# Kernel optimization log

Hardware: AMD Instinct MI355X
Metric: run time of the kernel (lower is better)

## Reference

```python
import jax, jax.numpy as jnp
import numpy as np

EPS = 1e-8

def setup_inputs() -> dict:
    key = jax.random.key(0)
    k1, k2 = jax.random.split(key)
    B, C, T_text, max_len = 16, 256, 512, 4096
    x = jax.random.normal(k1, (B, C, T_text), dtype=jnp.float32)
    # positive linear-domain durations, mean ~ max_len / T_text = 8
    w = jax.random.uniform(k2, (B, T_text), dtype=jnp.float32) * 16.0
    x_mask = jnp.ones((B, 1, T_text), dtype=jnp.float32)
    y_mask = jnp.ones((B, 1, max_len), dtype=jnp.float32)
    sigma_scale = jnp.ones((1,), dtype=jnp.float32)
    return {"x": x, "w": w, "x_mask": x_mask, "y_mask": y_mask, "sigma_scale": sigma_scale}

def reference(x, w, x_mask, y_mask, sigma_scale):
    # x: (B, C, T_text), w: (B, T_text), y_mask: (B, 1, max_len)
    x = x * x_mask
    center = jnp.cumsum(w, axis=1) - 0.5 * w            # (B, T_text)
    max_len = y_mask.shape[2]
    pos = jnp.arange(max_len, dtype=x.dtype)            # (max_len,)
    mu = pos[None, None, :] - center[:, :, None]        # (B, T_text, max_len)
    sigma = w[:, :, None] * sigma_scale[0]              # (B, T_text, 1)
    weights = jnp.exp(-0.5 * jnp.square(mu) / (jnp.square(sigma) + EPS))
    weights = weights / (jnp.sum(weights, axis=1, keepdims=True) + EPS)
    upsampled = jnp.einsum('bct,btl->bcl', x, weights)  # (B, C, max_len)
    return upsampled * y_mask
```

## Files before the change

### kernel.cpp

```cpp
#include <hip/hip_runtime.h>
#include <hip/hip_bf16.h>

#define EPS 1e-8f

#define BB 16
#define CC 256
#define TT 512
#define LL 4096
#define KC  32
#define TCB 128
#define TLB 64
#define XR  40

typedef __attribute__((ext_vector_type(8))) short short8;
typedef __attribute__((ext_vector_type(4))) float f32x4;

__device__ __forceinline__ unsigned short bfbits(float f) {
    __hip_bfloat16 h = __float2bfloat16(f);
    return *(unsigned short*)&h;
}
__device__ __forceinline__ unsigned int pack2(float lo, float hi) {
    return (unsigned int)bfbits(lo) | ((unsigned int)bfbits(hi) << 16);
}

__global__ __launch_bounds__(512)
void scan_kernel(const float* __restrict__ w,
                 const float* __restrict__ sigma_scale,
                 float* __restrict__ center,
                 float* __restrict__ nhis,
                 float* __restrict__ delta) {
    const int b = blockIdx.x;
    const int t = threadIdx.x;
    const int lane = t & 63;
    const int wid  = t >> 6;
    __shared__ float part[8], offs[8], wmx[8];

    const float wv = w[b * TT + t];
    float v = wv;
#pragma unroll
    for (int o = 1; o < 64; o <<= 1) {
        float u = __shfl_up(v, o);
        if (lane >= o) v += u;
    }
    float m = wv;
#pragma unroll
    for (int o = 1; o < 64; o <<= 1) m = fmaxf(m, __shfl_xor(m, o));
    if (lane == 63) part[wid] = v;
    if (lane == 0)  wmx[wid] = m;
    __syncthreads();
    const float ss = sigma_scale[0];
    if (t == 0) {
        float run = 0.0f, mm = 0.0f;
#pragma unroll
        for (int i = 0; i < 8; ++i) {
            offs[i] = run;
            run += part[i];
            mm = fmaxf(mm, wmx[i]);
        }
        delta[b] = 8.0f * (mm * ss + 1e-4f) + 1.0f;
    }
    __syncthreads();
    v += offs[wid];
    center[b * TT + t] = v - 0.5f * wv;
    const float sg = wv * ss;
    nhis[b * TT + t] = -0.5f / (sg * sg + EPS);
}


#define ISSUE(tc_)                                                              \
    {                                                                           \
        _Pragma("unroll")                                                       \
        for (int i = 0; i < 4; ++i) {                                           \
            const int idx4 = tid + 256 * i;                                     \
            const int c    = idx4 >> 3;                                         \
            const int t4   = idx4 & 7;                                          \
            gx[i] = *(const float4*)&x[xbase + (size_t)c * TT + (tc_) + t4 * 4];\
        }                                                                       \
    }

#define WRITEX(buf_)                                                            \
    {                                                                           \
        _Pragma("unroll")                                                       \
        for (int i = 0; i < 4; ++i) {                                           \
            const int idx4 = tid + 256 * i;                                     \
            const int c    = idx4 >> 3;                                         \
            const int t4   = idx4 & 7;                                          \
            ushort4 v4;                                                         \
            v4.x = bfbits(gx[i].x);                                             \
            v4.y = bfbits(gx[i].y);                                             \
            v4.z = bfbits(gx[i].z);                                             \
            v4.w = bfbits(gx[i].w);                                             \
            *(ushort4*)&xs[buf_][c][t4 * 4] = v4;                               \
        }                                                                       \
    }

#define EXPW(tc_, buf_)                                                         \
    {                                                                           \
        _Pragma("unroll")                                                       \
        for (int i = 0; i < 2; ++i) {                                           \
            const int slot  = tid + 256 * i;                                    \
            const int l_loc = slot >> 3;                                        \
            const int t4    = slot & 7;                                         \
            const int t0    = (tc_) + t4 * 4;                                   \
            const float4 cv = *(const float4*)&center[bTT + t0];                \
            const float4 nv = *(const float4*)&nhis[bTT + t0];                  \
            const float4 xm = *(const float4*)&x_mask[bTT + t0];                \
            const float posf = (float)(l0 + l_loc);                             \
            float mu, e0, e1, e2, e3;                                           \
            mu = posf - cv.x; e0 = __expf(mu * mu * nv.x);                      \
            mu = posf - cv.y; e1 = __expf(mu * mu * nv.y);                      \
            mu = posf - cv.z; e2 = __expf(mu * mu * nv.z);                      \
            mu = posf - cv.w; e3 = __expf(mu * mu * nv.w);                      \
            const float ps = (e0 + e1) + (e2 + e3);                             \
            if (i == 0) p0 += ps; else p1 += ps;                                \
            uint2 pk;                                                           \
            pk.x = pack2(e0 * xm.x, e1 * xm.y);                                 \
            pk.y = pack2(e2 * xm.z, e3 * xm.w);                                 \
            *(uint2*)&ws[buf_][l_loc][t4 * 4] = pk;                             \
        }                                                                       \
    }

#define MFMA_STEP(buf_)                                                         \
    {                                                                           \
        short8 af[2], bfr[4];                                                   \
        _Pragma("unroll")                                                       \
        for (int m = 0; m < 2; ++m)                                             \
            af[m] = *(const short8*)&xs[buf_][wv * 32 + m * 16 + lq][lg * 8];   \
        _Pragma("unroll")                                                       \
        for (int n = 0; n < 4; ++n)                                             \
            bfr[n] = *(const short8*)&ws[buf_][n * 16 + lq][lg * 8];            \
        _Pragma("unroll")                                                       \
        for (int m = 0; m < 2; ++m)                                             \
            _Pragma("unroll")                                                   \
            for (int n = 0; n < 4; ++n)                                         \
                acc[m][n] = __builtin_amdgcn_mfma_f32_16x16x32_bf16(            \
                    af[m], bfr[n], acc[m][n], 0, 0, 0);                         \
    }

__global__ __launch_bounds__(256, 4)
void fused_kernel(const float* __restrict__ x,
                  const float* __restrict__ x_mask,
                  const float* __restrict__ y_mask,
                  const float* __restrict__ center,
                  const float* __restrict__ nhis,
                  const float* __restrict__ delta,
                  float* __restrict__ out) {
    __shared__ unsigned short xs[2][TCB][XR];
    __shared__ unsigned short ws[2][TLB][XR];
    __shared__ float dsum[TLB];
    __shared__ float sscale[TLB];
    __shared__ int tmin_s, tmax_s;

    const int gid = blockIdx.x;
    const int lid = (gid & 7) * 256 + (gid >> 3);
    const int b   = lid >> 7;
    const int rr_ = lid & 127;
    const int l0  = (rr_ >> 1) * TLB;
    const int c0  = (rr_ & 1) * TCB;

    const int tid  = threadIdx.x;
    const int lane = tid & 63;
    const int wv   = tid >> 6;
    const int lq   = lane & 15;
    const int lg   = lane >> 4;
    const int bTT  = b * TT;
    const size_t xbase = (size_t)(b * CC + c0) * TT;

    if (tid == 0) { tmin_s = TT; tmax_s = -1; }
    __syncthreads();
    const float D  = delta[b];
    const float lo = (float)l0 - D;
    const float hi = (float)(l0 + TLB - 1) + D;
#pragma unroll
    for (int i = 0; i < 2; ++i) {
        const int tt = tid + 256 * i;
        const float c = center[bTT + tt];
        if (c >= lo && c <= hi) {
            atomicMin(&tmin_s, tt);
            atomicMax(&tmax_s, tt);
        }
    }
    __syncthreads();
    const int tlo = tmin_s & ~(KC - 1);
    const int nch = (tmax_s >= 0) ? ((((tmax_s & ~(KC - 1)) + KC) - tlo) / KC) : 0;

    f32x4 acc[2][4];
#pragma unroll
    for (int m = 0; m < 2; ++m)
#pragma unroll
        for (int n = 0; n < 4; ++n) acc[m][n] = (f32x4)0.0f;
    float p0 = 0.0f, p1 = 0.0f;

    float4 gx[4];

    if (nch > 0) {
        ISSUE(tlo);
        EXPW(tlo, 0);
        WRITEX(0);
        __syncthreads();
        for (int i = 0; i < nch; ++i) {
            const int cur = i & 1;
            const int tc1 = tlo + (i + 1) * KC;
            if (i + 1 < nch) {
                ISSUE(tc1);
                EXPW(tc1, cur ^ 1);
            }
            MFMA_STEP(cur);
            if (i + 1 < nch) WRITEX(cur ^ 1);
            __syncthreads();
        }
    }

#pragma unroll
    for (int o = 1; o < 8; o <<= 1) {
        p0 += __shfl_xor(p0, o);
        p1 += __shfl_xor(p1, o);
    }
    if ((tid & 7) == 0) {
        dsum[tid >> 3]        = p0;
        dsum[(tid >> 3) + 32] = p1;
    }
    __syncthreads();
    if (tid < TLB)
        sscale[tid] = y_mask[b * LL + l0 + tid] / (dsum[tid] + EPS);
    __syncthreads();

    float sc[4];
#pragma unroll
    for (int n = 0; n < 4; ++n) sc[n] = sscale[n * 16 + lq];

    const size_t obase = (size_t)(b * CC + c0) * LL + l0;
#pragma unroll
    for (int m = 0; m < 2; ++m) {
#pragma unroll
        for (int r = 0; r < 4; ++r) {
            const int c = wv * 32 + m * 16 + lg * 4 + r;
            float* op = &out[obase + (size_t)c * LL];
#pragma unroll
            for (int n = 0; n < 4; ++n)
                op[n * 16 + lq] = acc[m][n][r] * sc[n];
        }
    }
}

extern "C" void kernel_launch(void* const* d_in, const int* in_sizes, int n_in,
                              void* d_out, int out_size, void* d_ws, size_t ws_size,
                              hipStream_t stream) {
    const float* x           = (const float*)d_in[0];
    const float* w           = (const float*)d_in[1];
    const float* x_mask      = (const float*)d_in[2];
    const float* y_mask      = (const float*)d_in[3];
    const float* sigma_scale = (const float*)d_in[4];
    float* out = (float*)d_out;

    float* center = (float*)d_ws;
    float* nhis   = center + BB * TT;
    float* delta  = nhis + BB * TT;

    hipLaunchKernelGGL(scan_kernel, dim3(BB), dim3(512), 0, stream,
                       w, sigma_scale, center, nhis, delta);
    hipLaunchKernelGGL(fused_kernel, dim3((LL / TLB) * (CC / TCB) * BB), dim3(256), 0, stream,
                       x, x_mask, y_mask, center, nhis, delta, out);
}
```

Before: 28.30 us.

## Fuse scan into main kernel, widen L tile, load x fragments directly from global

Drops the separate scan kernel: each block recomputes the prefix sum, centers, inverse variances and delta for its batch row in shared memory, removing one launch and the global round trip for the intermediates. The L tile doubles to 128, so each wave holds 16 accumulators and the grid halves. The x tile is no longer staged through shared memory; each lane reads its MFMA A fragment straight from global memory and converts it to bf16. The risks are redundant scan work in every block, more register pressure, and exposed global-load latency inside the MFMA loop.

Result: faster. 24.29 us (-14.2%).

```diff
diff --git a/kernel.cpp b/kernel.cpp
--- a/kernel.cpp
+++ b/kernel.cpp
@@ -9,7 +9,7 @@
 #define LL 4096
 #define KC  32
 #define TCB 128
-#define TLB 64
+#define TLB 128
 #define XR  40
 
 typedef __attribute__((ext_vector_type(8))) short short8;
@@ -23,223 +23,191 @@
     return (unsigned int)bfbits(lo) | ((unsigned int)bfbits(hi) << 16);
 }
 
-__global__ __launch_bounds__(512)
-void scan_kernel(const float* __restrict__ w,
-                 const float* __restrict__ sigma_scale,
-                 float* __restrict__ center,
-                 float* __restrict__ nhis,
-                 float* __restrict__ delta) {
-    const int b = blockIdx.x;
-    const int t = threadIdx.x;
-    const int lane = t & 63;
-    const int wid  = t >> 6;
-    __shared__ float part[8], offs[8], wmx[8];
-
-    const float wv = w[b * TT + t];
-    float v = wv;
+
+#define EXPW(tc_, buf_)                                                         \
+    {                                                                           \
+        _Pragma("unroll")                                                       \
+        for (int i_ = 0; i_ < 2; ++i_) {                                        \
+            const int slot  = tid + 256 * i_;                                   \
+            const int l_loc = slot >> 2;                                        \
+            const int tg    = slot & 3;                                         \
+            const int t0    = (tc_) + tg * 8;                                   \
+            const float4 cv0 = *(const float4*)&cen_s[t0];                      \
+            const float4 cv1 = *(const float4*)&cen_s[t0 + 4];                  \
+            const float4 nv0 = *(const float4*)&nh_s[t0];                       \
+            const float4 nv1 = *(const float4*)&nh_s[t0 + 4];                   \
+            const float4 xk0 = *(const float4*)&xm_s[t0];                       \
+            const float4 xk1 = *(const float4*)&xm_s[t0 + 4];                   \
+            const float posf = (float)(l0 + l_loc);                             \
+            float mu, e0, e1, e2, e3, e4, e5, e6, e7;                           \
+            mu = posf - cv0.x; e0 = __expf(mu * mu * nv0.x);                    \
+            mu = posf - cv0.y; e1 = __expf(mu * mu * nv0.y);                    \
+            mu = posf - cv0.z; e2 = __expf(mu * mu * nv0.z);                    \
+            mu = posf - cv0.w; e3 = __expf(mu * mu * nv0.w);                    \
+            mu = posf - cv1.x; e4 = __expf(mu * mu * nv1.x);                    \
+            mu = posf - cv1.y; e5 = __expf(mu * mu * nv1.y);                    \
+            mu = posf - cv1.z; e6 = __expf(mu * mu * nv1.z);                    \
+            mu = posf - cv1.w; e7 = __expf(mu * mu * nv1.w);                    \
+            const float ps = ((e0 + e1) + (e2 + e3)) + ((e4 + e5) + (e6 + e7)); \
+            if (i_ == 0) p0 += ps; else p1 += ps;                               \
+            uint4 pk;                                                           \
+            pk.x = pack2(e0 * xk0.x, e1 * xk0.y);                               \
+            pk.y = pack2(e2 * xk0.z, e3 * xk0.w);                               \
+            pk.z = pack2(e4 * xk1.x, e5 * xk1.y);                               \
+            pk.w = pack2(e6 * xk1.z, e7 * xk1.w);                               \
+            *(uint4*)&ws[buf_][l_loc][tg * 8] = pk;                             \
+        }                                                                       \
+    }
+
+#define AFRAG(AF, crow_, tc_)                                                   \
+    {                                                                           \
+        const float* xp = &x[xbase + (size_t)(crow_) * TT + (tc_) + lg * 8];    \
+        const float4 a0 = *(const float4*)xp;                                   \
+        const float4 a1 = *(const float4*)(xp + 4);                             \
+        uint4 ap;                                                               \
+        ap.x = pack2(a0.x, a0.y);                                               \
+        ap.y = pack2(a0.z, a0.w);                                               \
+        ap.z = pack2(a1.x, a1.y);                                               \
+        ap.w = pack2(a1.z, a1.w);                                               \
+        AF = *(short8*)&ap;                                                     \
+    }
+
+#define MFMA_STEP(buf_, tc_)                                                    \
+    {                                                                           \
+        short8 af0, af1;                                                        \
+        AFRAG(af0, wv * 32 + lq, tc_);                                          \
+        AFRAG(af1, wv * 32 + 16 + lq, tc_);                                     \
+        _Pragma("unroll")                                                       \
+        for (int n = 0; n < 8; ++n) {                                           \
+            const short8 bfr = *(const short8*)&ws[buf_][n * 16 + lq][lg * 8];  \
+            acc0[n] = __builtin_amdgcn_mfma_f32_16x16x32_bf16(af0, bfr, acc0[n], 0, 0, 0); \
+            acc1[n] = __builtin_amdgcn_mfma_f32_16x16x32_bf16(af1, bfr, acc1[n], 0, 0, 0); \
+        }                                                                       \
+    }
+
+__global__ __launch_bounds__(256, 4)
+void fused_kernel(const float* __restrict__ x,
+                  const float* __restrict__ w,
+                  const float* __restrict__ x_mask,
+                  const float* __restrict__ y_mask,
+                  const float* __restrict__ sigma_scale,
+                  float* __restrict__ out) {
+    __shared__ unsigned short ws[2][TLB][XR];
+    __shared__ float cen_s[TT], nh_s[TT], xm_s[TT];
+    __shared__ float dsum[TLB], sscale[TLB];
+    __shared__ float part[4], wmx[4], offs[4];
+    __shared__ float sdelta;
+    __shared__ int tmin_s, tmax_s;
+
+    const int gid = blockIdx.x;
+    const int lid = (gid & 7) * 128 + (gid >> 3);
+    const int b   = lid >> 6;
+    const int rr  = lid & 63;
+    const int l0  = (rr >> 1) * TLB;
+    const int c0  = (rr & 1) * TCB;
+
+    const int tid  = threadIdx.x;
+    const int lane = tid & 63;
+    const int wid  = tid >> 6;
+    const int wv   = wid;
+    const int lq   = lane & 15;
+    const int lg   = lane >> 4;
+    const int bTT  = b * TT;
+    const size_t xbase = (size_t)(b * CC + c0) * TT;
+
+    if (tid == 0) { tmin_s = TT; tmax_s = -1; }
+
+    const int t2 = tid * 2;
+    const float2 w2  = *(const float2*)&w[bTT + t2];
+    const float2 xm2 = *(const float2*)&x_mask[bTT + t2];
+    const float ss = sigma_scale[0];
+    const float pairsum = w2.x + w2.y;
+    float v = pairsum;
 #pragma unroll
     for (int o = 1; o < 64; o <<= 1) {
         float u = __shfl_up(v, o);
         if (lane >= o) v += u;
     }
-    float m = wv;
-#pragma unroll
-    for (int o = 1; o < 64; o <<= 1) m = fmaxf(m, __shfl_xor(m, o));
+    float pm = fmaxf(w2.x, w2.y);
+#pragma unroll
+    for (int o = 1; o < 64; o <<= 1) pm = fmaxf(pm, __shfl_xor(pm, o));
     if (lane == 63) part[wid] = v;
-    if (lane == 0)  wmx[wid] = m;
-    __syncthreads();
-    const float ss = sigma_scale[0];
-    if (t == 0) {
+    if (lane == 0)  wmx[wid] = pm;
+    __syncthreads();
+    if (tid == 0) {
         float run = 0.0f, mm = 0.0f;
 #pragma unroll
-        for (int i = 0; i < 8; ++i) {
+        for (int i = 0; i < 4; ++i) {
             offs[i] = run;
             run += part[i];
             mm = fmaxf(mm, wmx[i]);
         }
-        delta[b] = 8.0f * (mm * ss + 1e-4f) + 1.0f;
-    }
-    __syncthreads();
-    v += offs[wid];
-    center[b * TT + t] = v - 0.5f * wv;
-    const float sg = wv * ss;
-    nhis[b * TT + t] = -0.5f / (sg * sg + EPS);
-}
-
-
-#define ISSUE(tc_)                                                              \
-    {                                                                           \
-        _Pragma("unroll")                                                       \
-        for (int i = 0; i < 4; ++i) {                                           \
-            const int idx4 = tid + 256 * i;                                     \
-            const int c    = idx4 >> 3;                                         \
-            const int t4   = idx4 & 7;                                          \
-            gx[i] = *(const float4*)&x[xbase + (size_t)c * TT + (tc_) + t4 * 4];\
-        }                                                                       \
-    }
-
-#define WRITEX(buf_)                                                            \
-    {                                                                           \
-        _Pragma("unroll")                                                       \
-        for (int i = 0; i < 4; ++i) {                                           \
-            const int idx4 = tid + 256 * i;                                     \
-            const int c    = idx4 >> 3;                                         \
-            const int t4   = idx4 & 7;                                          \
-            ushort4 v4;                                                         \
-            v4.x = bfbits(gx[i].x);                                             \
-            v4.y = bfbits(gx[i].y);                                             \
-            v4.z = bfbits(gx[i].z);                                             \
-            v4.w = bfbits(gx[i].w);                                             \
-            *(ushort4*)&xs[buf_][c][t4 * 4] = v4;                               \
-        }                                                                       \
-    }
-
-#define EXPW(tc_, buf_)                                                         \
-    {                                                                           \
-        _Pragma("unroll")                                                       \
-        for (int i = 0; i < 2; ++i) {                                           \
-            const int slot  = tid + 256 * i;                                    \
-            const int l_loc = slot >> 3;                                        \
-            const int t4    = slot & 7;                                         \
-            const int t0    = (tc_) + t4 * 4;                                   \
-            const float4 cv = *(const float4*)&center[bTT + t0];                \
-            const float4 nv = *(const float4*)&nhis[bTT + t0];                  \
-            const float4 xm = *(const float4*)&x_mask[bTT + t0];                \
-            const float posf = (float)(l0 + l_loc);                             \
-            float mu, e0, e1, e2, e3;                                           \
-            mu = posf - cv.x; e0 = __expf(mu * mu * nv.x);                      \
-            mu = posf - cv.y; e1 = __expf(mu * mu * nv.y);                      \
-            mu = posf - cv.z; e2 = __expf(mu * mu * nv.z);                      \
-            mu = posf - cv.w; e3 = __expf(mu * mu * nv.w);                      \
-            const float ps = (e0 + e1) + (e2 + e3);                             \
-            if (i == 0) p0 += ps; else p1 += ps;                                \
-            uint2 pk;                                                           \
-            pk.x = pack2(e0 * xm.x, e1 * xm.y);                                 \
-            pk.y = pack2(e2 * xm.z, e3 * xm.w);                                 \
-            *(uint2*)&ws[buf_][l_loc][t4 * 4] = pk;                             \
-        }                                                                       \
-    }
-
-#define MFMA_STEP(buf_)                                                         \
-    {                                                                           \
-        short8 af[2], bfr[4];                                                   \
-        _Pragma("unroll")                                                       \
-        for (int m = 0; m < 2; ++m)                                             \
-            af[m] = *(const short8*)&xs[buf_][wv * 32 + m * 16 + lq][lg * 8];   \
-        _Pragma("unroll")                                                       \
-        for (int n = 0; n < 4; ++n)                                             \
-            bfr[n] = *(const short8*)&ws[buf_][n * 16 + lq][lg * 8];            \
-        _Pragma("unroll")                                                       \
-        for (int m = 0; m < 2; ++m)                                             \
-            _Pragma("unroll")                                                   \
-            for (int n = 0; n < 4; ++n)                                         \
-                acc[m][n] = __builtin_amdgcn_mfma_f32_16x16x32_bf16(            \
-                    af[m], bfr[n], acc[m][n], 0, 0, 0);                         \
-    }
-
-__global__ __launch_bounds__(256, 4)
-void fused_kernel(const float* __restrict__ x,
-                  const float* __restrict__ x_mask,
-                  const float* __restrict__ y_mask,
-                  const float* __restrict__ center,
-                  const float* __restrict__ nhis,
-                  const float* __restrict__ delta,
-                  float* __restrict__ out) {
-    __shared__ unsigned short xs[2][TCB][XR];
-    __shared__ unsigned short ws[2][TLB][XR];
-    __shared__ float dsum[TLB];
-    __shared__ float sscale[TLB];
-    __shared__ int tmin_s, tmax_s;
-
-    const int gid = blockIdx.x;
-    const int lid = (gid & 7) * 256 + (gid >> 3);
-    const int b   = lid >> 7;
-    const int rr_ = lid & 127;
-    const int l0  = (rr_ >> 1) * TLB;
-    const int c0  = (rr_ & 1) * TCB;
-
-    const int tid  = threadIdx.x;
-    const int lane = tid & 63;
-    const int wv   = tid >> 6;
-    const int lq   = lane & 15;
-    const int lg   = lane >> 4;
-    const int bTT  = b * TT;
-    const size_t xbase = (size_t)(b * CC + c0) * TT;
-
-    if (tid == 0) { tmin_s = TT; tmax_s = -1; }
-    __syncthreads();
-    const float D  = delta[b];
+        sdelta = 8.0f * (mm * ss + 1e-4f) + 1.0f;
+    }
+    __syncthreads();
+    const float base = offs[wid] + v - pairsum;
+    const float cum1 = base + w2.x;
+    const float cum2 = cum1 + w2.y;
+    const float cenA = cum1 - 0.5f * w2.x;
+    const float cenB = cum2 - 0.5f * w2.y;
+    cen_s[t2]     = cenA;
+    cen_s[t2 + 1] = cenB;
+    const float sgA = w2.x * ss, sgB = w2.y * ss;
+    nh_s[t2]     = -0.5f / (sgA * sgA + EPS);
+    nh_s[t2 + 1] = -0.5f / (sgB * sgB + EPS);
+    xm_s[t2]     = xm2.x;
+    xm_s[t2 + 1] = xm2.y;
+
+    const float D  = sdelta;
     const float lo = (float)l0 - D;
     const float hi = (float)(l0 + TLB - 1) + D;
-#pragma unroll
-    for (int i = 0; i < 2; ++i) {
-        const int tt = tid + 256 * i;
-        const float c = center[bTT + tt];
-        if (c >= lo && c <= hi) {
-            atomicMin(&tmin_s, tt);
-            atomicMax(&tmax_s, tt);
-        }
-    }
+    if (cenA >= lo && cenA <= hi) { atomicMin(&tmin_s, t2);     atomicMax(&tmax_s, t2); }
+    if (cenB >= lo && cenB <= hi) { atomicMin(&tmin_s, t2 + 1); atomicMax(&tmax_s, t2 + 1); }
     __syncthreads();
     const int tlo = tmin_s & ~(KC - 1);
     const int nch = (tmax_s >= 0) ? ((((tmax_s & ~(KC - 1)) + KC) - tlo) / KC) : 0;
 
-    f32x4 acc[2][4];
-#pragma unroll
-    for (int m = 0; m < 2; ++m)
-#pragma unroll
-        for (int n = 0; n < 4; ++n) acc[m][n] = (f32x4)0.0f;
+    f32x4 acc0[8], acc1[8];
+#pragma unroll
+    for (int n = 0; n < 8; ++n) { acc0[n] = (f32x4)0.0f; acc1[n] = (f32x4)0.0f; }
     float p0 = 0.0f, p1 = 0.0f;
 
-    float4 gx[4];
-
     if (nch > 0) {
-        ISSUE(tlo);
         EXPW(tlo, 0);
-        WRITEX(0);
         __syncthreads();
         for (int i = 0; i < nch; ++i) {
             const int cur = i & 1;
-            const int tc1 = tlo + (i + 1) * KC;
-            if (i + 1 < nch) {
-                ISSUE(tc1);
-                EXPW(tc1, cur ^ 1);
-            }
-            MFMA_STEP(cur);
-            if (i + 1 < nch) WRITEX(cur ^ 1);
+            if (i + 1 < nch) EXPW(tlo + (i + 1) * KC, cur ^ 1);
+            MFMA_STEP(cur, tlo + i * KC);
             __syncthreads();
         }
     }
 
-#pragma unroll
-    for (int o = 1; o < 8; o <<= 1) {
-        p0 += __shfl_xor(p0, o);
-        p1 += __shfl_xor(p1, o);
-    }
-    if ((tid & 7) == 0) {
-        dsum[tid >> 3]        = p0;
-        dsum[(tid >> 3) + 32] = p1;
+    p0 += __shfl_xor(p0, 1); p0 += __shfl_xor(p0, 2);
+    p1 += __shfl_xor(p1, 1); p1 += __shfl_xor(p1, 2);
+    if ((tid & 3) == 0) {
+        dsum[tid >> 2]        = p0;
+        dsum[(tid >> 2) + 64] = p1;
     }
     __syncthreads();
     if (tid < TLB)
         sscale[tid] = y_mask[b * LL + l0 + tid] / (dsum[tid] + EPS);
     __syncthreads();
 
-    float sc[4];
-#pragma unroll
-    for (int n = 0; n < 4; ++n) sc[n] = sscale[n * 16 + lq];
+    float sc[8];
+#pragma unroll
+    for (int n = 0; n < 8; ++n) sc[n] = sscale[n * 16 + lq];
 
     const size_t obase = (size_t)(b * CC + c0) * LL + l0;
 #pragma unroll
-    for (int m = 0; m < 2; ++m) {
-#pragma unroll
-        for (int r = 0; r < 4; ++r) {
-            const int c = wv * 32 + m * 16 + lg * 4 + r;
-            float* op = &out[obase + (size_t)c * LL];
-#pragma unroll
-            for (int n = 0; n < 4; ++n)
-                op[n * 16 + lq] = acc[m][n][r] * sc[n];
-        }
+    for (int r = 0; r < 4; ++r) {
+        const int cA = wv * 32 + lg * 4 + r;
+        float* opA = &out[obase + (size_t)cA * LL];
+#pragma unroll
+        for (int n = 0; n < 8; ++n) opA[n * 16 + lq] = acc0[n][r] * sc[n];
+        float* opB = opA + 16 * LL;
+#pragma unroll
+        for (int n = 0; n < 8; ++n) opB[n * 16 + lq] = acc1[n][r] * sc[n];
     }
 }
 
@@ -253,12 +221,6 @@
     const float* sigma_scale = (const float*)d_in[4];
     float* out = (float*)d_out;
 
-    float* center = (float*)d_ws;
-    float* nhis   = center + BB * TT;
-    float* delta  = nhis + BB * TT;
-
-    hipLaunchKernelGGL(scan_kernel, dim3(BB), dim3(512), 0, stream,
-                       w, sigma_scale, center, nhis, delta);
     hipLaunchKernelGGL(fused_kernel, dim3((LL / TLB) * (CC / TCB) * BB), dim3(256), 0, stream,
-                       x, x_mask, y_mask, center, nhis, delta, out);
-}
+                       x, w, x_mask, y_mask, sigma_scale, out);
+}
```
